# Kernel optimization log

Hardware: AMD Instinct MI355X
Metric: run time of the kernel (lower is better)

## Reference

```python
import jax, jax.numpy as jnp
import numpy as np


def gcn_conv(x, src, dst, deg_inv_sqrt, W, b, n_nodes):
    # PyG GCNConv: linear transform first, then normalized aggregation (A_hat = D^-1/2 (A+I) D^-1/2)
    h = x @ W                                   # [N, out]
    norm = deg_inv_sqrt[src] * deg_inv_sqrt[dst]  # [E+N]
    msg = h[src] * norm[:, None]                # gather + scale
    out = jax.ops.segment_sum(msg, dst, num_segments=n_nodes)
    return out + b


def setup_inputs() -> dict:
    key = jax.random.key(0)
    ks = jax.random.split(key, 10)
    N, E, D_in, D_h = 50000, 640000, 128, 64
    x = jax.random.normal(ks[0], (N, D_in), dtype=jnp.float32)
    edge_index = jax.random.randint(ks[1], (2, E), 0, N, dtype=jnp.int64)

    def glorot(k, fan_in, fan_out):
        lim = jnp.sqrt(6.0 / (fan_in + fan_out)).astype(jnp.float32)
        return jax.random.uniform(k, (fan_in, fan_out), jnp.float32, -lim, lim)

    return {
        "x": x,
        "edge_index": edge_index,
        "W1": glorot(ks[2], D_in, D_h), "b1": jnp.zeros((D_h,), jnp.float32),
        "W2": glorot(ks[3], D_h, D_h),  "b2": jnp.zeros((D_h,), jnp.float32),
        "W3": glorot(ks[4], D_h, D_h),  "b3": jnp.zeros((D_h,), jnp.float32),
        "W4": glorot(ks[5], D_h, D_in), "b4": jnp.zeros((D_in,), jnp.float32),
    }


def reference(x, edge_index, W1, b1, W2, b2, W3, b3, W4, b4):
    n = x.shape[0]
    loops = jnp.arange(n, dtype=edge_index.dtype)
    src = jnp.concatenate([edge_index[0], loops])  # A + I self-loops
    dst = jnp.concatenate([edge_index[1], loops])
    deg = jax.ops.segment_sum(jnp.ones_like(dst, dtype=x.dtype), dst, num_segments=n)
    deg_inv_sqrt = jnp.where(deg > 0, jax.lax.rsqrt(deg), 0.0)

    h = jax.nn.relu(gcn_conv(x, src, dst, deg_inv_sqrt, W1, b1, n))
    # dropout is identity in eval mode
    z = jax.nn.relu(gcn_conv(h, src, dst, deg_inv_sqrt, W2, b2, n))
    x_hat = jax.nn.relu(gcn_conv(z, src, dst, deg_inv_sqrt, W3, b3, n))
    x_hat = gcn_conv(x_hat, src, dst, deg_inv_sqrt, W4, b4, n)
    return (x_hat, z)
```

## Files before the change

kernel.cpp:

```cpp
#include <hip/hip_runtime.h>
#include <hip/hip_bf16.h>



__global__ __launch_bounds__(256) void init_k(int* __restrict__ deg, int Npad) {
    int i = blockIdx.x * 256 + threadIdx.x;
    if (i < Npad) deg[i] = 0;
}

__global__ __launch_bounds__(256) void hist_deg(const int* __restrict__ dst,
                                                int* __restrict__ deg, int E) {
    int e = blockIdx.x * 256 + threadIdx.x;
    if (e < E) atomicAdd(&deg[dst[e]], 1);
}

__global__ __launch_bounds__(256) void scan_phase1(const int* __restrict__ deg,
                                                   int* __restrict__ block_sums) {
    int b = blockIdx.x, t = threadIdx.x;
    const int4* p = reinterpret_cast<const int4*>(deg + (size_t)b * 2048);
    int4 a = p[t * 2], c = p[t * 2 + 1];
    int s = a.x + a.y + a.z + a.w + c.x + c.y + c.z + c.w;
#pragma unroll
    for (int off = 32; off; off >>= 1) s += __shfl_down(s, off);
    __shared__ int wsum[4];
    if ((t & 63) == 0) wsum[t >> 6] = s;
    __syncthreads();
    if (t == 0) block_sums[b] = wsum[0] + wsum[1] + wsum[2] + wsum[3];
}

__global__ __launch_bounds__(256) void scan_phase2(const int* __restrict__ block_sums,
                                                   int* __restrict__ block_off,
                                                   int* __restrict__ row_ptr,
                                                   int B, int N) {
    __shared__ int s[256];
    int t = threadIdx.x;
    int v = (t < B) ? block_sums[t] : 0;
    s[t] = v;
    __syncthreads();
#pragma unroll
    for (int off = 1; off < 256; off <<= 1) {
        int u = (t >= off) ? s[t - off] : 0;
        __syncthreads();
        s[t] += u;
        __syncthreads();
    }
    if (t < B) block_off[t] = s[t] - v;
    if (t == 255) row_ptr[N] = s[255];
}

__global__ __launch_bounds__(256) void scan_phase3(const int* __restrict__ deg,
                                                   const int* __restrict__ block_off,
                                                   int* __restrict__ row_ptr,
                                                   float* __restrict__ dis, int N) {
    int b = blockIdx.x, t = threadIdx.x;
    int base = b * 2048 + t * 8;
    const int4* p = reinterpret_cast<const int4*>(deg + base);
    int4 a = p[0], c = p[1];
    int d[8] = {a.x, a.y, a.z, a.w, c.x, c.y, c.z, c.w};
    int pre[8], s = 0;
#pragma unroll
    for (int j = 0; j < 8; ++j) { pre[j] = s; s += d[j]; }
    __shared__ int ls[256];
    ls[t] = s;
    __syncthreads();
#pragma unroll
    for (int off = 1; off < 256; off <<= 1) {
        int u = (t >= off) ? ls[t - off] : 0;
        __syncthreads();
        ls[t] += u;
        __syncthreads();
    }
    int excl = ls[t] - s + block_off[b];
#pragma unroll
    for (int j = 0; j < 8; ++j) {
        int i = base + j;
        if (i < N) {
            row_ptr[i] = excl + pre[j];
            dis[i] = rsqrtf((float)(d[j] + 1));
        }
    }
}

__global__ __launch_bounds__(256) void fill_csr(const int* __restrict__ src,
                                                const int* __restrict__ dst,
                                                const int* __restrict__ row_ptr,
                                                int* __restrict__ deg,
                                                int* __restrict__ csr_src, int E) {
    int e = blockIdx.x * 256 + threadIdx.x;
    if (e < E) {
        int d = dst[e];
        int old = atomicSub(&deg[d], 1);
        csr_src[row_ptr[d] + old - 1] = src[e];
    }
}


__device__ __forceinline__ ushort r16(float f) {
    __hip_bfloat16 h = __float2bfloat16(f);
    return *reinterpret_cast<ushort*>(&h);
}
__device__ __forceinline__ float bf_lo(unsigned u) {
    return __builtin_bit_cast(float, u << 16);
}
__device__ __forceinline__ float bf_hi(unsigned u) {
    return __builtin_bit_cast(float, u & 0xFFFF0000u);
}

__device__ __forceinline__ void gather_pair_u(const unsigned* __restrict__ G,
                                              const int* __restrict__ csr_src,
                                              int begA, int lenA,
                                              int begB, int lenB,
                                              int lane, int h, int fl,
                                              float& loA_o, float& hiA_o,
                                              float& loB_o, float& hiB_o) {
    int idxA = 0, idxB = 0;
    if (lenA > 0) idxA = csr_src[begA + (lane < lenA ? lane : lenA - 1)];
    if (lenB > 0) idxB = csr_src[begB + (lane < lenB ? lane : lenB - 1)];

    int cA = lenA < 64 ? lenA : 64;
    int cB = lenB < 64 ? lenB : 64;
    int pA = (cA + 1) >> 1;
    int pB = (cB + 1) >> 1;
    int pM = pA > pB ? pA : pB;

    float lA[4] = {0.f, 0.f, 0.f, 0.f}, hA[4] = {0.f, 0.f, 0.f, 0.f};
    float lB[4] = {0.f, 0.f, 0.f, 0.f}, hB[4] = {0.f, 0.f, 0.f, 0.f};

    for (int k = 0; k < pM; k += 8) {
        unsigned uA[8], uB[8];
        int ee[8];
#pragma unroll
        for (int i = 0; i < 8; ++i) {
            int e = h + 2 * (k + i);
            ee[i] = e;
            int sA = __shfl(idxA, e);
            int sB = __shfl(idxB, e);
            uA[i] = G[(unsigned)sA * 32u + fl];
            uB[i] = G[(unsigned)sB * 32u + fl];
        }
#pragma unroll
        for (int i = 0; i < 8; ++i) {
            unsigned a = (ee[i] < cA) ? uA[i] : 0u;
            unsigned b = (ee[i] < cB) ? uB[i] : 0u;
            lA[i & 3] += bf_lo(a);  hA[i & 3] += bf_hi(a);
            lB[i & 3] += bf_lo(b);  hB[i & 3] += bf_hi(b);
        }
    }
    for (int e2 = 64 + h; e2 < lenA; e2 += 2) {
        unsigned u = G[(unsigned)csr_src[begA + e2] * 32u + fl];
        lA[0] += bf_lo(u); hA[0] += bf_hi(u);
    }
    for (int e2 = 64 + h; e2 < lenB; e2 += 2) {
        unsigned u = G[(unsigned)csr_src[begB + e2] * 32u + fl];
        lB[0] += bf_lo(u); hB[0] += bf_hi(u);
    }

    float lo = (lA[0] + lA[1]) + (lA[2] + lA[3]);
    float hi = (hA[0] + hA[1]) + (hA[2] + hA[3]);
    lo += __shfl_xor(lo, 32);
    hi += __shfl_xor(hi, 32);
    loA_o = lo;  hiA_o = hi;
    float lob = (lB[0] + lB[1]) + (lB[2] + lB[3]);
    float hib = (hB[0] + hB[1]) + (hB[2] + hB[3]);
    lob += __shfl_xor(lob, 32);
    hib += __shfl_xor(hib, 32);
    loB_o = lob;  hiB_o = hib;
}

template <int K, int DOUT>
__global__ __launch_bounds__(256) void gemm_scale(const float* __restrict__ A,
                                                  const float* __restrict__ W,
                                                  const float* __restrict__ dis,
                                                  ushort* __restrict__ G16, int N) {
    constexpr int CG   = DOUT / 4;
    constexpr int RG   = 256 / CG;
    constexpr int ROWS = RG * 4;
    constexpr int LDA  = K + 4;

    __shared__ __align__(16) float a_lds[ROWS * LDA];
    __shared__ __align__(16) float w_lds[K * DOUT];

    int t    = threadIdx.x;
    int row0 = blockIdx.x * ROWS;

    constexpr int WF4 = K * DOUT / 4;
    for (int q = t; q < WF4; q += 256)
        reinterpret_cast<float4*>(w_lds)[q] =
            reinterpret_cast<const float4*>(W)[q];

    constexpr int AF4 = ROWS * K / 4;
    for (int q = t; q < AF4; q += 256) {
        int r  = q / (K / 4);
        int kc = q % (K / 4);
        float4 v = make_float4(0.f, 0.f, 0.f, 0.f);
        int gr = row0 + r;
        if (gr < N)
            v = reinterpret_cast<const float4*>(A + (size_t)gr * K)[kc];
        *reinterpret_cast<float4*>(&a_lds[r * LDA + kc * 4]) = v;
    }
    __syncthreads();

    int c0 = (t % CG) * 4;
    int r0 = (t / CG) * 4;

    float4 acc[4] = {};
#pragma unroll 1
    for (int k = 0; k < K; k += 4) {
        float4 w0 = *reinterpret_cast<const float4*>(&w_lds[(k + 0) * DOUT + c0]);
        float4 w1 = *reinterpret_cast<const float4*>(&w_lds[(k + 1) * DOUT + c0]);
        float4 w2 = *reinterpret_cast<const float4*>(&w_lds[(k + 2) * DOUT + c0]);
        float4 w3 = *reinterpret_cast<const float4*>(&w_lds[(k + 3) * DOUT + c0]);
#pragma unroll
        for (int j = 0; j < 4; ++j) {
            float4 a4 = *reinterpret_cast<const float4*>(&a_lds[(r0 + j) * LDA + k]);
            acc[j].x += a4.x * w0.x + a4.y * w1.x + a4.z * w2.x + a4.w * w3.x;
            acc[j].y += a4.x * w0.y + a4.y * w1.y + a4.z * w2.y + a4.w * w3.y;
            acc[j].z += a4.x * w0.z + a4.y * w1.z + a4.z * w2.z + a4.w * w3.z;
            acc[j].w += a4.x * w0.w + a4.y * w1.w + a4.z * w2.w + a4.w * w3.w;
        }
    }

#pragma unroll
    for (int j = 0; j < 4; ++j) {
        int gr = row0 + r0 + j;
        if (gr < N) {
            float s = dis[gr];
            float4 o = acc[j];
            ushort4 pk;
            pk.x = r16(o.x * s); pk.y = r16(o.y * s);
            pk.z = r16(o.z * s); pk.w = r16(o.w * s);
            *reinterpret_cast<ushort4*>(&G16[(size_t)gr * DOUT + c0]) = pk;
        }
    }
}

template <int K, int DOUT>
__global__ __launch_bounds__(256) void gemm_bias(const float* __restrict__ A,
                                                 const float* __restrict__ W,
                                                 const float* __restrict__ bias,
                                                 float* __restrict__ Out, int N) {
    constexpr int CG   = DOUT / 4;
    constexpr int RG   = 256 / CG;
    constexpr int ROWS = RG * 4;
    constexpr int LDA  = K + 4;

    __shared__ __align__(16) float a_lds[ROWS * LDA];
    __shared__ __align__(16) float w_lds[K * DOUT];

    int t    = threadIdx.x;
    int row0 = blockIdx.x * ROWS;

    constexpr int WF4 = K * DOUT / 4;
    for (int q = t; q < WF4; q += 256)
        reinterpret_cast<float4*>(w_lds)[q] =
            reinterpret_cast<const float4*>(W)[q];

    constexpr int AF4 = ROWS * K / 4;
    for (int q = t; q < AF4; q += 256) {
        int r  = q / (K / 4);
        int kc = q % (K / 4);
        float4 v = make_float4(0.f, 0.f, 0.f, 0.f);
        int gr = row0 + r;
        if (gr < N)
            v = reinterpret_cast<const float4*>(A + (size_t)gr * K)[kc];
        *reinterpret_cast<float4*>(&a_lds[r * LDA + kc * 4]) = v;
    }
    __syncthreads();

    int c0 = (t % CG) * 4;
    int r0 = (t / CG) * 4;

    float4 acc[4] = {};
#pragma unroll 1
    for (int k = 0; k < K; k += 4) {
        float4 w0 = *reinterpret_cast<const float4*>(&w_lds[(k + 0) * DOUT + c0]);
        float4 w1 = *reinterpret_cast<const float4*>(&w_lds[(k + 1) * DOUT + c0]);
        float4 w2 = *reinterpret_cast<const float4*>(&w_lds[(k + 2) * DOUT + c0]);
        float4 w3 = *reinterpret_cast<const float4*>(&w_lds[(k + 3) * DOUT + c0]);
#pragma unroll
        for (int j = 0; j < 4; ++j) {
            float4 a4 = *reinterpret_cast<const float4*>(&a_lds[(r0 + j) * LDA + k]);
            acc[j].x += a4.x * w0.x + a4.y * w1.x + a4.z * w2.x + a4.w * w3.x;
            acc[j].y += a4.x * w0.y + a4.y * w1.y + a4.z * w2.y + a4.w * w3.y;
            acc[j].z += a4.x * w0.z + a4.y * w1.z + a4.z * w2.z + a4.w * w3.z;
            acc[j].w += a4.x * w0.w + a4.y * w1.w + a4.z * w2.w + a4.w * w3.w;
        }
    }

    float4 b4v = *reinterpret_cast<const float4*>(&bias[c0]);
#pragma unroll
    for (int j = 0; j < 4; ++j) {
        int gr = row0 + r0 + j;
        if (gr < N) {
            float4 o = acc[j];
            o.x += b4v.x; o.y += b4v.y; o.z += b4v.z; o.w += b4v.w;
            reinterpret_cast<float4*>(Out + (size_t)gr * DOUT)[c0 / 4] = o;
        }
    }
}

template <bool WRITE_F32>
__global__ __launch_bounds__(256) void agg_gemm_pair(
    const unsigned* __restrict__ G,
    const int* __restrict__ row_ptr,
    const int* __restrict__ csr_src,
    const float* __restrict__ dis,
    const float* __restrict__ bias,
    const float* __restrict__ Wn,
    unsigned* __restrict__ Gout,
    float* __restrict__ Zout,
    int N) {
    __shared__ __align__(16) float w_lds[64 * 64];
    __shared__ __align__(16) float a_buf[4][2][64];

    int t = threadIdx.x;
    for (int q = t; q < 64 * 64 / 4; q += 256)
        reinterpret_cast<float4*>(w_lds)[q] =
            reinterpret_cast<const float4*>(Wn)[q];
    __syncthreads();

    int wave = t >> 6, lane = t & 63;
    int h = lane >> 5, fl = lane & 31;

    int n0 = (blockIdx.x * 4 + wave) * 2;
    if (n0 >= N) return;
    int n1 = n0 + 1;
    bool hasB = (n1 < N);
    int n1c = hasB ? n1 : n0;
    int nn = h ? n1c : n0;

    int begA = row_ptr[n0];
    int endA = row_ptr[n0 + 1];
    int lenA = endA - begA;
    int begB = 0, lenB = 0;
    if (hasB) { begB = endA; lenB = row_ptr[n0 + 2] - endA; }

    float dn0 = dis[n0], dn1 = dis[n1c];
    unsigned us = G[(unsigned)nn * 32u + fl];
    float2 b2 = reinterpret_cast<const float2*>(bias)[fl];

    float loA, hiA, loB, hiB;
    gather_pair_u(G, csr_src, begA, lenA, begB, lenB, lane, h, fl,
                  loA, hiA, loB, hiB);

    float dn = h ? dn1 : dn0;
    float lo = h ? loB : loA;
    float hi = h ? hiB : hiA;
    float vlo = fmaxf(dn * (lo + bf_lo(us)) + b2.x, 0.f);
    float vhi = fmaxf(dn * (hi + bf_hi(us)) + b2.y, 0.f);

    *reinterpret_cast<float2*>(&a_buf[wave][h][2 * fl]) = make_float2(vlo, vhi);
    if (WRITE_F32 && (h == 0 || hasB))
        reinterpret_cast<float2*>(Zout)[(size_t)nn * 32 + fl] =
            make_float2(vlo, vhi);

    __builtin_amdgcn_wave_barrier();

    float yA0 = 0.f, yA1 = 0.f, yA2 = 0.f, yA3 = 0.f;
    float yB0 = 0.f, yB1 = 0.f, yB2 = 0.f, yB3 = 0.f;
    for (int k = 0; k < 64; k += 4) {
        float4 a4 = *reinterpret_cast<const float4*>(&a_buf[wave][0][k]);
        float4 c4 = *reinterpret_cast<const float4*>(&a_buf[wave][1][k]);
        float w0 = w_lds[(k + 0) * 64 + lane];
        float w1 = w_lds[(k + 1) * 64 + lane];
        float w2 = w_lds[(k + 2) * 64 + lane];
        float w3 = w_lds[(k + 3) * 64 + lane];
        yA0 += a4.x * w0; yA1 += a4.y * w1; yA2 += a4.z * w2; yA3 += a4.w * w3;
        yB0 += c4.x * w0; yB1 += c4.y * w1; yB2 += c4.z * w2; yB3 += c4.w * w3;
    }
    float yA = (yA0 + yA1) + (yA2 + yA3);
    float yB = (yB0 + yB1) + (yB2 + yB3);

    float l0 = __shfl(yA, 2 * fl), h0 = __shfl(yA, 2 * fl + 1);
    float l1 = __shfl(yB, 2 * fl), h1 = __shfl(yB, 2 * fl + 1);
    float yl = h ? l1 : l0;
    float yh = h ? h1 : h0;
    if (h == 0 || hasB) {
        unsigned pk = (unsigned)r16(dn * yl) | ((unsigned)r16(dn * yh) << 16);
        Gout[(unsigned)nn * 32u + fl] = pk;
    }
}

__global__ __launch_bounds__(256) void aggregate_s3(const unsigned* __restrict__ G,
                                                    const int* __restrict__ row_ptr,
                                                    const int* __restrict__ csr_src,
                                                    const float* __restrict__ dis,
                                                    const float* __restrict__ bias,
                                                    unsigned* __restrict__ Out, int N) {
    int t = threadIdx.x;
    int wave = t >> 6, lane = t & 63;
    int h = lane >> 5, fl = lane & 31;

    int n0 = (blockIdx.x * 4 + wave) * 2;
    if (n0 >= N) return;
    int n1 = n0 + 1;
    bool hasB = (n1 < N);
    int n1c = hasB ? n1 : n0;
    int nn = h ? n1c : n0;

    int begA = row_ptr[n0];
    int endA = row_ptr[n0 + 1];
    int lenA = endA - begA;
    int begB = 0, lenB = 0;
    if (hasB) { begB = endA; lenB = row_ptr[n0 + 2] - endA; }

    float dn0 = dis[n0], dn1 = dis[n1c];
    unsigned us = G[(unsigned)nn * 32u + fl];
    float2 b2 = reinterpret_cast<const float2*>(bias)[fl];

    float loA, hiA, loB, hiB;
    gather_pair_u(G, csr_src, begA, lenA, begB, lenB, lane, h, fl,
                  loA, hiA, loB, hiB);

    float dn = h ? dn1 : dn0;
    float lo = h ? loB : loA;
    float hi = h ? hiB : hiA;
    float vlo = fmaxf(dn * (lo + bf_lo(us)) + b2.x, 0.f);
    float vhi = fmaxf(dn * (hi + bf_hi(us)) + b2.y, 0.f);

    if (h == 0 || hasB) {
        unsigned pk = (unsigned)r16(dn * vlo) | ((unsigned)r16(dn * vhi) << 16);
        Out[(unsigned)nn * 32u + fl] = pk;
    }
}

__global__ __launch_bounds__(256) void aggregate_t(const unsigned* __restrict__ G,
                                                   const int* __restrict__ row_ptr,
                                                   const int* __restrict__ csr_src,
                                                   const float* __restrict__ dis,
                                                   float* __restrict__ Out, int N) {
    int t = threadIdx.x;
    int wave = t >> 6, lane = t & 63;
    int h = lane >> 5, fl = lane & 31;

    int n0 = (blockIdx.x * 4 + wave) * 2;
    if (n0 >= N) return;
    int n1 = n0 + 1;
    bool hasB = (n1 < N);
    int n1c = hasB ? n1 : n0;
    int nn = h ? n1c : n0;

    int begA = row_ptr[n0];
    int endA = row_ptr[n0 + 1];
    int lenA = endA - begA;
    int begB = 0, lenB = 0;
    if (hasB) { begB = endA; lenB = row_ptr[n0 + 2] - endA; }

    float dn0 = dis[n0], dn1 = dis[n1c];
    unsigned us = G[(unsigned)nn * 32u + fl];

    float loA, hiA, loB, hiB;
    gather_pair_u(G, csr_src, begA, lenA, begB, lenB, lane, h, fl,
                  loA, hiA, loB, hiB);

    float dn = h ? dn1 : dn0;
    float lo = h ? loB : loA;
    float hi = h ? hiB : hiA;

    if (h == 0 || hasB)
        reinterpret_cast<float2*>(Out)[(size_t)nn * 32 + fl] =
            make_float2(dn * (lo + bf_lo(us)), dn * (hi + bf_hi(us)));
}


extern "C" void kernel_launch(void* const* d_in, const int* in_sizes, int n_in,
                              void* d_out, int out_size, void* d_ws, size_t ws_size,
                              hipStream_t stream) {
    const float* x     = (const float*)d_in[0];
    const int*   edges = (const int*)d_in[1];
    const float* W1 = (const float*)d_in[2];
    const float* b1 = (const float*)d_in[3];
    const float* W2 = (const float*)d_in[4];
    const float* b2 = (const float*)d_in[5];
    const float* W3 = (const float*)d_in[6];
    const float* b3 = (const float*)d_in[7];
    const float* W4 = (const float*)d_in[8];
    const float* b4 = (const float*)d_in[9];

    const int DIN = 128, DH = 64;
    int N = in_sizes[0] / DIN;
    int E = in_sizes[1] / 2;

    const int* e_src = edges;
    const int* e_dst = edges + E;

    float* out   = (float*)d_out;
    float* x_hat = out;
    float* z     = out + (size_t)N * DIN;

    int B    = (N + 2047) / 2048;
    int Npad = B * 2048;

    char*  ws  = (char*)d_ws;
    size_t woff = 0;
    auto carve = [&](size_t bytes) {
        void* p = ws + woff;
        woff = (woff + bytes + 255) & ~(size_t)255;
        return p;
    };
    float*    dis        = (float*)   carve((size_t)N * 4);
    int*      deg        = (int*)     carve((size_t)Npad * 4);
    int*      row_ptr    = (int*)     carve((size_t)(N + 1) * 4);
    int*      csr_src    = (int*)     carve((size_t)E * 4);
    int*      block_sums = (int*)     carve((size_t)B * 4);
    int*      block_off  = (int*)     carve((size_t)B * 4);
    unsigned* gA         = (unsigned*)carve((size_t)N * DH * 2);
    unsigned* gB         = (unsigned*)carve((size_t)N * DH * 2);
    float*    t          = (float*)   carve((size_t)N * DH * 4);
    (void)ws_size;

    int nb_e = (E + 255) / 256;
    int nb_p = (N + 7) / 8;

    init_k<<<(Npad + 255) / 256, 256, 0, stream>>>(deg, Npad);
    hist_deg<<<nb_e, 256, 0, stream>>>(e_dst, deg, E);
    scan_phase1<<<B, 256, 0, stream>>>(deg, block_sums);
    scan_phase2<<<1, 256, 0, stream>>>(block_sums, block_off, row_ptr, B, N);
    scan_phase3<<<B, 256, 0, stream>>>(deg, block_off, row_ptr, dis, N);
    fill_csr<<<nb_e, 256, 0, stream>>>(e_src, e_dst, row_ptr, deg, csr_src, E);

    gemm_scale<128, 64><<<(N + 63) / 64, 256, 0, stream>>>(
        x, W1, dis, (ushort*)gA, N);

    agg_gemm_pair<false><<<nb_p, 256, 0, stream>>>(
        gA, row_ptr, csr_src, dis, b1, W2, gB, nullptr, N);

    agg_gemm_pair<true><<<nb_p, 256, 0, stream>>>(
        gB, row_ptr, csr_src, dis, b2, W3, gA, z, N);

    aggregate_s3<<<nb_p, 256, 0, stream>>>(
        gA, row_ptr, csr_src, dis, b3, gB, N);

    aggregate_t<<<nb_p, 256, 0, stream>>>(
        gB, row_ptr, csr_src, dis, t, N);
    gemm_bias<64, 128><<<(N + 31) / 32, 256, 0, stream>>>(t, W4, b4, x_hat, N);
}
```

Before: 298.7 us.

## Remap gather lanes to 16-lane groups with 8-byte bf16 loads per edge

Rewrites the neighbour gather so each 16-lane group loads 4 bf16 features (uint2) per edge, with four groups covering two nodes × two edge parities. Before, each half-wave issued 4-byte loads and every lane gathered rows for both nodes. The new mapping halves the number of load instructions per row and removes the duplicated gather for the sibling node, at the cost of a 32-edge first pass instead of 64 and more work in the tail loop for high-degree nodes. Stores are widened to float4 or uint2, and only one group per node writes results.

```diff
diff --git a/kernel.cpp b/kernel.cpp
--- a/kernel.cpp
+++ b/kernel.cpp
@@ -106,65 +106,71 @@
     return __builtin_bit_cast(float, u & 0xFFFF0000u);
 }
 
-__device__ __forceinline__ void gather_pair_u(const unsigned* __restrict__ G,
-                                              const int* __restrict__ csr_src,
-                                              int begA, int lenA,
-                                              int begB, int lenB,
-                                              int lane, int h, int fl,
-                                              float& loA_o, float& hiA_o,
-                                              float& loB_o, float& hiB_o) {
+__device__ __forceinline__ void gather_pair_u2(const unsigned* __restrict__ G,
+                                               const int* __restrict__ csr_src,
+                                               int begA, int lenA,
+                                               int begB, int lenB, int lane,
+                                               float& s0o, float& s1o,
+                                               float& s2o, float& s3o) {
+    int l32 = lane & 31;
     int idxA = 0, idxB = 0;
-    if (lenA > 0) idxA = csr_src[begA + (lane < lenA ? lane : lenA - 1)];
-    if (lenB > 0) idxB = csr_src[begB + (lane < lenB ? lane : lenB - 1)];
-
-    int cA = lenA < 64 ? lenA : 64;
-    int cB = lenB < 64 ? lenB : 64;
-    int pA = (cA + 1) >> 1;
-    int pB = (cB + 1) >> 1;
-    int pM = pA > pB ? pA : pB;
-
-    float lA[4] = {0.f, 0.f, 0.f, 0.f}, hA[4] = {0.f, 0.f, 0.f, 0.f};
-    float lB[4] = {0.f, 0.f, 0.f, 0.f}, hB[4] = {0.f, 0.f, 0.f, 0.f};
+    if (lenA > 0) idxA = csr_src[begA + (l32 < lenA ? l32 : lenA - 1)];
+    if (lenB > 0) idxB = csr_src[begB + (l32 < lenB ? l32 : lenB - 1)];
+
+    int grp     = lane >> 4;
+    int p       = grp & 1;
+    int nodeSel = grp >> 1;
+    int f       = lane & 15;
+
+    int cA = lenA < 32 ? lenA : 32;
+    int cB = lenB < 32 ? lenB : 32;
+    int cOwn = nodeSel ? cB : cA;
+    int cM = cA > cB ? cA : cB;
+    int pM = (cM + 1) >> 1;
+
+    float a0 = 0.f, a1 = 0.f, a2 = 0.f, a3 = 0.f;
+    float b0 = 0.f, b1 = 0.f, b2 = 0.f, b3 = 0.f;
 
     for (int k = 0; k < pM; k += 8) {
-        unsigned uA[8], uB[8];
+        uint2 u[8];
         int ee[8];
 #pragma unroll
         for (int i = 0; i < 8; ++i) {
-            int e = h + 2 * (k + i);
+            int e = p + 2 * (k + i);
             ee[i] = e;
             int sA = __shfl(idxA, e);
             int sB = __shfl(idxB, e);
-            uA[i] = G[(unsigned)sA * 32u + fl];
-            uB[i] = G[(unsigned)sB * 32u + fl];
+            int s = nodeSel ? sB : sA;
+            u[i] = *reinterpret_cast<const uint2*>(G + (unsigned)s * 32u + 2 * f);
         }
 #pragma unroll
         for (int i = 0; i < 8; ++i) {
-            unsigned a = (ee[i] < cA) ? uA[i] : 0u;
-            unsigned b = (ee[i] < cB) ? uB[i] : 0u;
-            lA[i & 3] += bf_lo(a);  hA[i & 3] += bf_hi(a);
-            lB[i & 3] += bf_lo(b);  hB[i & 3] += bf_hi(b);
-        }
-    }
-    for (int e2 = 64 + h; e2 < lenA; e2 += 2) {
-        unsigned u = G[(unsigned)csr_src[begA + e2] * 32u + fl];
-        lA[0] += bf_lo(u); hA[0] += bf_hi(u);
-    }
-    for (int e2 = 64 + h; e2 < lenB; e2 += 2) {
-        unsigned u = G[(unsigned)csr_src[begB + e2] * 32u + fl];
-        lB[0] += bf_lo(u); hB[0] += bf_hi(u);
-    }
-
-    float lo = (lA[0] + lA[1]) + (lA[2] + lA[3]);
-    float hi = (hA[0] + hA[1]) + (hA[2] + hA[3]);
-    lo += __shfl_xor(lo, 32);
-    hi += __shfl_xor(hi, 32);
-    loA_o = lo;  hiA_o = hi;
-    float lob = (lB[0] + lB[1]) + (lB[2] + lB[3]);
-    float hib = (hB[0] + hB[1]) + (hB[2] + hB[3]);
-    lob += __shfl_xor(lob, 32);
-    hib += __shfl_xor(hib, 32);
-    loB_o = lob;  hiB_o = hib;
+            unsigned ux = (ee[i] < cOwn) ? u[i].x : 0u;
+            unsigned uy = (ee[i] < cOwn) ? u[i].y : 0u;
+            if (i & 1) {
+                b0 += bf_lo(ux); b1 += bf_hi(ux);
+                b2 += bf_lo(uy); b3 += bf_hi(uy);
+            } else {
+                a0 += bf_lo(ux); a1 += bf_hi(ux);
+                a2 += bf_lo(uy); a3 += bf_hi(uy);
+            }
+        }
+    }
+    int begOwn = nodeSel ? begB : begA;
+    int lenOwn = nodeSel ? lenB : lenA;
+    for (int e2 = 32 + p; e2 < lenOwn; e2 += 2) {
+        int s = csr_src[begOwn + e2];
+        uint2 v = *reinterpret_cast<const uint2*>(G + (unsigned)s * 32u + 2 * f);
+        a0 += bf_lo(v.x); a1 += bf_hi(v.x);
+        a2 += bf_lo(v.y); a3 += bf_hi(v.y);
+    }
+
+    float r0 = a0 + b0, r1 = a1 + b1, r2 = a2 + b2, r3 = a3 + b3;
+    r0 += __shfl_xor(r0, 16);
+    r1 += __shfl_xor(r1, 16);
+    r2 += __shfl_xor(r2, 16);
+    r3 += __shfl_xor(r3, 16);
+    s0o = r0; s1o = r1; s2o = r2; s3o = r3;
 }
 
 template <int K, int DOUT>
@@ -321,6 +327,7 @@
 
     int wave = t >> 6, lane = t & 63;
     int h = lane >> 5, fl = lane & 31;
+    int grp = lane >> 4, f = lane & 15;
 
     int n0 = (blockIdx.x * 4 + wave) * 2;
     if (n0 >= N) return;
@@ -336,23 +343,24 @@
     if (hasB) { begB = endA; lenB = row_ptr[n0 + 2] - endA; }
 
     float dn0 = dis[n0], dn1 = dis[n1c];
-    unsigned us = G[(unsigned)nn * 32u + fl];
-    float2 b2 = reinterpret_cast<const float2*>(bias)[fl];
-
-    float loA, hiA, loB, hiB;
-    gather_pair_u(G, csr_src, begA, lenA, begB, lenB, lane, h, fl,
-                  loA, hiA, loB, hiB);
+    uint2 us2 = *reinterpret_cast<const uint2*>(G + (size_t)nn * 32 + 2 * f);
+    float4 b4 = reinterpret_cast<const float4*>(bias)[f];
+
+    float s0, s1, s2, s3;
+    gather_pair_u2(G, csr_src, begA, lenA, begB, lenB, lane, s0, s1, s2, s3);
 
     float dn = h ? dn1 : dn0;
-    float lo = h ? loB : loA;
-    float hi = h ? hiB : hiA;
-    float vlo = fmaxf(dn * (lo + bf_lo(us)) + b2.x, 0.f);
-    float vhi = fmaxf(dn * (hi + bf_hi(us)) + b2.y, 0.f);
-
-    *reinterpret_cast<float2*>(&a_buf[wave][h][2 * fl]) = make_float2(vlo, vhi);
-    if (WRITE_F32 && (h == 0 || hasB))
-        reinterpret_cast<float2*>(Zout)[(size_t)nn * 32 + fl] =
-            make_float2(vlo, vhi);
+    float v0 = fmaxf(dn * (s0 + bf_lo(us2.x)) + b4.x, 0.f);
+    float v1 = fmaxf(dn * (s1 + bf_hi(us2.x)) + b4.y, 0.f);
+    float v2 = fmaxf(dn * (s2 + bf_lo(us2.y)) + b4.z, 0.f);
+    float v3 = fmaxf(dn * (s3 + bf_hi(us2.y)) + b4.w, 0.f);
+
+    if ((grp & 1) == 0)
+        *reinterpret_cast<float4*>(&a_buf[wave][h][4 * f]) =
+            make_float4(v0, v1, v2, v3);
+    if (WRITE_F32 && (grp == 0 || (grp == 2 && hasB)))
+        *reinterpret_cast<float4*>(Zout + (size_t)nn * 64 + 4 * f) =
+            make_float4(v0, v1, v2, v3);
 
     __builtin_amdgcn_wave_barrier();
 
@@ -389,7 +397,8 @@
                                                     unsigned* __restrict__ Out, int N) {
     int t = threadIdx.x;
     int wave = t >> 6, lane = t & 63;
-    int h = lane >> 5, fl = lane & 31;
+    int h = lane >> 5;
+    int grp = lane >> 4, f = lane & 15;
 
     int n0 = (blockIdx.x * 4 + wave) * 2;
     if (n0 >= N) return;
@@ -405,22 +414,23 @@
     if (hasB) { begB = endA; lenB = row_ptr[n0 + 2] - endA; }
 
     float dn0 = dis[n0], dn1 = dis[n1c];
-    unsigned us = G[(unsigned)nn * 32u + fl];
-    float2 b2 = reinterpret_cast<const float2*>(bias)[fl];
-
-    float loA, hiA, loB, hiB;
-    gather_pair_u(G, csr_src, begA, lenA, begB, lenB, lane, h, fl,
-                  loA, hiA, loB, hiB);
+    uint2 us2 = *reinterpret_cast<const uint2*>(G + (size_t)nn * 32 + 2 * f);
+    float4 b4 = reinterpret_cast<const float4*>(bias)[f];
+
+    float s0, s1, s2, s3;
+    gather_pair_u2(G, csr_src, begA, lenA, begB, lenB, lane, s0, s1, s2, s3);
 
     float dn = h ? dn1 : dn0;
-    float lo = h ? loB : loA;
-    float hi = h ? hiB : hiA;
-    float vlo = fmaxf(dn * (lo + bf_lo(us)) + b2.x, 0.f);
-    float vhi = fmaxf(dn * (hi + bf_hi(us)) + b2.y, 0.f);
-
-    if (h == 0 || hasB) {
-        unsigned pk = (unsigned)r16(dn * vlo) | ((unsigned)r16(dn * vhi) << 16);
-        Out[(unsigned)nn * 32u + fl] = pk;
+    float o0 = fmaxf(dn * (s0 + bf_lo(us2.x)) + b4.x, 0.f);
+    float o1 = fmaxf(dn * (s1 + bf_hi(us2.x)) + b4.y, 0.f);
+    float o2 = fmaxf(dn * (s2 + bf_lo(us2.y)) + b4.z, 0.f);
+    float o3 = fmaxf(dn * (s3 + bf_hi(us2.y)) + b4.w, 0.f);
+
+    if (grp == 0 || (grp == 2 && hasB)) {
+        uint2 pk2;
+        pk2.x = (unsigned)r16(dn * o0) | ((unsigned)r16(dn * o1) << 16);
+        pk2.y = (unsigned)r16(dn * o2) | ((unsigned)r16(dn * o3) << 16);
+        *reinterpret_cast<uint2*>(Out + (size_t)nn * 32 + 2 * f) = pk2;
     }
 }
 
@@ -431,7 +441,8 @@
                                                    float* __restrict__ Out, int N) {
     int t = threadIdx.x;
     int wave = t >> 6, lane = t & 63;
-    int h = lane >> 5, fl = lane & 31;
+    int h = lane >> 5;
+    int grp = lane >> 4, f = lane & 15;
 
     int n0 = (blockIdx.x * 4 + wave) * 2;
     if (n0 >= N) return;
@@ -447,19 +458,16 @@
     if (hasB) { begB = endA; lenB = row_ptr[n0 + 2] - endA; }
 
     float dn0 = dis[n0], dn1 = dis[n1c];
-    unsigned us = G[(unsigned)nn * 32u + fl];
-
-    float loA, hiA, loB, hiB;
-    gather_pair_u(G, csr_src, begA, lenA, begB, lenB, lane, h, fl,
-                  loA, hiA, loB, hiB);
+    uint2 us2 = *reinterpret_cast<const uint2*>(G + (size_t)nn * 32 + 2 * f);
+
+    float s0, s1, s2, s3;
+    gather_pair_u2(G, csr_src, begA, lenA, begB, lenB, lane, s0, s1, s2, s3);
 
     float dn = h ? dn1 : dn0;
-    float lo = h ? loB : loA;
-    float hi = h ? hiB : hiA;
-
-    if (h == 0 || hasB)
-        reinterpret_cast<float2*>(Out)[(size_t)nn * 32 + fl] =
-            make_float2(dn * (lo + bf_lo(us)), dn * (hi + bf_hi(us)));
+    if (grp == 0 || (grp == 2 && hasB))
+        *reinterpret_cast<float4*>(Out + (size_t)nn * 64 + 4 * f) =
+            make_float4(dn * (s0 + bf_lo(us2.x)), dn * (s1 + bf_hi(us2.x)),
+                        dn * (s2 + bf_lo(us2.y)), dn * (s3 + bf_hi(us2.y)));
 }
 
 
```

After: 286.1 us. 1.04x faster.
